# Kernel optimization log

Measured on AMD Instinct MI355X. Metric: run time of the kernel, lower is better.

The kernel has to match this reference:

```python
import jax, jax.numpy as jnp
import numpy as np

N_NODES = 100000
N_EDGES = 400000
IN_DIM, HID, OUT_DIM, NUM_REL = 768, 256, 128, 3


def _init_linear(key, fan_in, fan_out):
    k1, k2 = jax.random.split(key)
    s = 1.0 / np.sqrt(fan_in)
    W = jax.random.uniform(k1, (fan_in, fan_out), jnp.float32, -s, s)
    b = jax.random.uniform(k2, (fan_out,), jnp.float32, -s, s)
    return W, b


def setup_inputs() -> dict:
    key = jax.random.key(0)
    ks = jax.random.split(key, 12)
    x = jax.random.normal(ks[0], (N_NODES, IN_DIM), jnp.float32)
    edge_index = jax.random.randint(ks[1], (2, N_EDGES), 0, N_NODES, jnp.int64 if jax.config.jax_enable_x64 else jnp.int32).astype(jnp.int32)
    edge_type = jax.random.randint(ks[2], (N_EDGES,), 0, NUM_REL).astype(jnp.int32)
    W1, b1 = _init_linear(ks[3], IN_DIM, HID)
    s = 1.0 / np.sqrt(HID)
    conv1_W = jax.random.uniform(ks[4], (NUM_REL, HID, HID), jnp.float32, -s, s)
    conv1_root = jax.random.uniform(ks[5], (HID, HID), jnp.float32, -s, s)
    conv1_bias = jnp.zeros((HID,), jnp.float32)
    conv2_W = jax.random.uniform(ks[6], (NUM_REL, HID, HID), jnp.float32, -s, s)
    conv2_root = jax.random.uniform(ks[7], (HID, HID), jnp.float32, -s, s)
    conv2_bias = jnp.zeros((HID,), jnp.float32)
    W2, b2 = _init_linear(ks[8], HID, OUT_DIM)
    Wc, bc = _init_linear(ks[9], OUT_DIM, 2)
    return {"x": x, "edge_index": edge_index, "edge_type": edge_type,
            "batch_size": 1024,
            "W1": W1, "b1": b1,
            "conv1_W": conv1_W, "conv1_root": conv1_root, "conv1_bias": conv1_bias,
            "conv2_W": conv2_W, "conv2_root": conv2_root, "conv2_bias": conv2_bias,
            "W2": W2, "b2": b2, "Wc": Wc, "bc": bc}


def rgcn_conv(h, src, dst, edge_type, W, root, bias):
    # PyG RGCNConv: mean aggregation per relation + root transform + bias
    n = h.shape[0]
    hs = h[src]                                   # [E, HID] gather
    out = h @ root + bias                         # root/self term
    for r in range(NUM_REL):                      # fixed small relation count
        w = (edge_type == r).astype(h.dtype)      # [E]
        msg = (hs @ W[r]) * w[:, None]            # per-relation transform
        ssum = jax.ops.segment_sum(msg, dst, num_segments=n)
        cnt = jax.ops.segment_sum(w, dst, num_segments=n)
        out = out + ssum / jnp.maximum(cnt, 1.0)[:, None]
    return out


def reference(x, edge_index, edge_type, batch_size,
              W1, b1, conv1_W, conv1_root, conv1_bias,
              conv2_W, conv2_root, conv2_bias, W2, b2, Wc, bc):
    src, dst = edge_index[0], edge_index[1]
    h = jax.nn.relu(x @ W1 + b1)                  # linear1 + ReLU
    h = rgcn_conv(h, src, dst, edge_type, conv1_W, conv1_root, conv1_bias)
    # dropout: identity at inference
    h = rgcn_conv(h, src, dst, edge_type, conv2_W, conv2_root, conv2_bias)
    h = jax.nn.relu(h @ W2 + b2)                  # linear2 + ReLU
    logits = h @ Wc + bc                          # classifier
    return logits[:batch_size]
```

## Files before the change

### kernel.cpp

```cpp
#include <hip/hip_runtime.h>


#define N_NODES 100000
#define N_EDGES 400000
#define IN_DIM  768
#define HID     256
#define OUT_DIM 128
#define NREL    3
#define BATCH   1024
#define KCAT    1024
#define MSGW    768
#define CAP0    32768
#define CAP1    8192
#define ECAP1   32768
#define ECAP2   8192

typedef __attribute__((ext_vector_type(8))) short bf16x8;
typedef __attribute__((ext_vector_type(4))) float f32x4;

static __device__ __forceinline__ int imin(int a, int b) { return a < b ? a : b; }

static __device__ __forceinline__ unsigned short f2bf(float f) {
    union { float f; unsigned int u; } v; v.f = f;
    unsigned int r = v.u + 0x7FFFu + ((v.u >> 16) & 1u);
    return (unsigned short)(r >> 16);
}

__global__ __launch_bounds__(256) void zero_prep(
    uint4* __restrict__ zp, int nz,
    const float* __restrict__ W1,
    const float* __restrict__ c1root, const float* __restrict__ c1W,
    const float* __restrict__ c2root, const float* __restrict__ c2W,
    unsigned short* __restrict__ w1s,
    unsigned short* __restrict__ B1s,
    unsigned short* __restrict__ B2s)
{
    int t = blockIdx.x * blockDim.x + threadIdx.x;
    if (t < nz) { zp[t] = make_uint4(0u, 0u, 0u, 0u); return; }
    int u = t - nz;
    const int P1 = (IN_DIM * HID) / 8;
    const int P2 = (KCAT * HID) / 8;
    unsigned int pk[4];
    if (u < P1) {
        int base = u * 8;
        int j0 = base & 31, c = (base >> 5) & 255, s = base >> 13;
        #pragma unroll
        for (int q = 0; q < 4; q++) {
            unsigned short lo = f2bf(W1[((s * 32 + j0 + 2 * q) << 8) + c]);
            unsigned short hi = f2bf(W1[((s * 32 + j0 + 2 * q + 1) << 8) + c]);
            pk[q] = (unsigned int)lo | ((unsigned int)hi << 16);
        }
        *(uint4*)&w1s[base] = make_uint4(pk[0], pk[1], pk[2], pk[3]);
    } else if (u < P1 + 2 * P2) {
        int which2 = (u - P1) >= P2;
        const float* root = which2 ? c2root : c1root;
        const float* Wr   = which2 ? c2W : c1W;
        unsigned short* dst = which2 ? B2s : B1s;
        int base = ((u - P1) - (which2 ? P2 : 0)) * 8;
        int j0 = base & 31, c = (base >> 5) & 255, s = base >> 13;
        int k0 = s * 32 + j0;
        #pragma unroll
        for (int q = 0; q < 4; q++) {
            int ka = k0 + 2 * q, kb = ka + 1;
            float va = (ka < HID) ? root[(ka << 8) + c] : Wr[((ka - HID) << 8) + c];
            float vb = (kb < HID) ? root[(kb << 8) + c] : Wr[((kb - HID) << 8) + c];
            pk[q] = (unsigned int)f2bf(va) | ((unsigned int)f2bf(vb) << 16);
        }
        *(uint4*)&dst[base] = make_uint4(pk[0], pk[1], pk[2], pk[3]);
    }
}


__global__ void mark1c(const int* __restrict__ ei, int* __restrict__ need1,
                       int* __restrict__ elist2, int* __restrict__ ectr2) {
    int e = blockIdx.x * blockDim.x + threadIdx.x;
    if (e >= N_EDGES) return;
    if (ei[N_EDGES + e] < BATCH) {
        need1[ei[e]] = 1;
        int p = atomicAdd(ectr2, 1);
        if (p < ECAP2) elist2[p] = e;
    }
}

__global__ void mark0c(const int* __restrict__ ei, const int* __restrict__ need1,
                       int* __restrict__ need0,
                       int* __restrict__ elist1, int* __restrict__ ectr1) {
    int e = blockIdx.x * blockDim.x + threadIdx.x;
    if (e >= N_EDGES) return;
    int d = ei[N_EDGES + e];
    if (d < BATCH || need1[d]) {
        need0[ei[e]] = 1;
        int p = atomicAdd(ectr1, 1);
        if (p < ECAP1) elist1[p] = e;
    }
}

__global__ void compact_both(const int* __restrict__ need1, const int* __restrict__ need0,
                             int* __restrict__ idx1, int* __restrict__ map1, int* __restrict__ n1ctr,
                             int* __restrict__ idx0, int* __restrict__ map0, int* __restrict__ n0ctr) {
    int i = blockIdx.x * blockDim.x + threadIdx.x;
    if (i >= N_NODES) return;
    int f1 = (i < BATCH) | need1[i];
    int f0 = f1 | need0[i];
    if (f1) {
        int p = atomicAdd(n1ctr, 1);
        if (p < CAP1) { idx1[p] = i; map1[i] = p; } else map1[i] = -1;
    } else map1[i] = -1;
    if (f0) {
        int p = atomicAdd(n0ctr, 1);
        if (p < CAP0) { idx0[p] = i; map0[i] = p; } else map0[i] = -1;
    } else map0[i] = -1;
}

__global__ void scatter_c(const int* __restrict__ ei, const int* __restrict__ et,
                          const int* __restrict__ elist, const int* __restrict__ ectr, int ecap,
                          const int* __restrict__ mapSrc, const int* __restrict__ mapDst,
                          const float* __restrict__ hsrc,
                          float* __restrict__ Amsg, float* __restrict__ cnt,
                          int cntStride) {
    int g = blockIdx.x * blockDim.x + threadIdx.x;
    int ii = g >> 6, lane = g & 63;
    int n = imin(*ectr, ecap);
    if (ii >= n) return;
    int e = elist[ii];
    int d = ei[N_EDGES + e];
    int row = mapDst ? mapDst[d] : d;
    if (row < 0) return;
    int s = mapSrc[ei[e]];
    if (s < 0) return;
    int r = et[e];
    float4 v = *(const float4*)(hsrc + (size_t)s * HID + lane * 4);
    float* dp = Amsg + (size_t)row * MSGW + (size_t)r * HID + lane * 4;
    atomicAdd(dp + 0, v.x);
    atomicAdd(dp + 1, v.y);
    atomicAdd(dp + 2, v.z);
    atomicAdd(dp + 3, v.w);
    if (lane == 0) atomicAdd(cnt + (size_t)r * cntStride + row, 1.0f);
}

__global__ __launch_bounds__(256) void gemm1_mfma(
    const float* __restrict__ x, const int* __restrict__ idx0,
    const unsigned short* __restrict__ w1s, const float* __restrict__ b1,
    float* __restrict__ h0c, const int* __restrict__ Mptr, int Mcap)
{
    int M = imin(*Mptr, Mcap);
    int bm = blockIdx.x * 64;
    if (bm >= M) return;

    __shared__ unsigned short As[64][40];
    __shared__ unsigned short Bs[256][40];

    int tid = threadIdx.x;
    int w = tid >> 6, lane = tid & 63;
    int l16 = lane & 15, lhi = lane >> 4;

    int ar = tid >> 2, ac = tid & 3;
    int gr = idx0[imin(bm + ar, M - 1)];
    const float* aptr = x + (size_t)gr * IN_DIM + ac * 8;

    f32x4 acc[16];
    #pragma unroll
    for (int i = 0; i < 16; i++) acc[i] = (f32x4)0.0f;

    for (int k0 = 0; k0 < IN_DIM; k0 += 32) {
        float4 a0 = *(const float4*)(aptr + k0);
        float4 a1 = *(const float4*)(aptr + k0 + 4);
        unsigned int p0 = (unsigned int)f2bf(a0.x) | ((unsigned int)f2bf(a0.y) << 16);
        unsigned int p1 = (unsigned int)f2bf(a0.z) | ((unsigned int)f2bf(a0.w) << 16);
        unsigned int p2 = (unsigned int)f2bf(a1.x) | ((unsigned int)f2bf(a1.y) << 16);
        unsigned int p3 = (unsigned int)f2bf(a1.z) | ((unsigned int)f2bf(a1.w) << 16);
        *(uint4*)&As[ar][ac * 8] = make_uint4(p0, p1, p2, p3);

        const uint4* bsrc = (const uint4*)(w1s + ((size_t)(k0 >> 5) * 256 + tid) * 32);
        int bswz = (tid >> 3) & 3;
        uint4 b0 = bsrc[0], b1v = bsrc[1], b2 = bsrc[2], b3 = bsrc[3];
        *(uint4*)&Bs[tid][(0 ^ bswz) * 8] = b0;
        *(uint4*)&Bs[tid][(1 ^ bswz) * 8] = b1v;
        *(uint4*)&Bs[tid][(2 ^ bswz) * 8] = b2;
        *(uint4*)&Bs[tid][(3 ^ bswz) * 8] = b3;
        __syncthreads();

        bf16x8 af = *(bf16x8*)&As[w * 16 + l16][lhi * 8];
        #pragma unroll
        for (int f = 0; f < 16; f++) {
            int col = f * 16 + l16;
            bf16x8 bf = *(bf16x8*)&Bs[col][(lhi ^ ((col >> 3) & 3)) * 8];
            acc[f] = __builtin_amdgcn_mfma_f32_16x16x32_bf16(af, bf, acc[f], 0, 0, 0);
        }
        __syncthreads();
    }

    #pragma unroll
    for (int f = 0; f < 16; f++) {
        int col = f * 16 + l16;
        float bb = b1[col];
        #pragma unroll
        for (int reg = 0; reg < 4; reg++) {
            int row = bm + w * 16 + lhi * 4 + reg;
            if (row < M) h0c[(size_t)row * HID + col] = fmaxf(acc[f][reg] + bb, 0.0f);
        }
    }
}

__global__ __launch_bounds__(256) void conv_mfma(
    const float* __restrict__ hsrc,
    const int* __restrict__ idx, const int* __restrict__ map,
    const float* __restrict__ Amsg,
    const float* __restrict__ cnt, int cntStride,
    const unsigned short* __restrict__ Bt, const float* __restrict__ bias,
    float* __restrict__ Cout, const int* __restrict__ Mptr, int Mcap)
{
    int M = Mptr ? imin(*Mptr, Mcap) : Mcap;
    int bm = blockIdx.x * 64;
    if (bm >= M) return;

    __shared__ unsigned short As[64][40];
    __shared__ unsigned short Bs[256][40];

    int tid = threadIdx.x;
    int w = tid >> 6, lane = tid & 63;
    int l16 = lane & 15, lhi = lane >> 4;

    int ar = tid >> 2, ac = tid & 3;
    int row = imin(bm + ar, M - 1);
    int node = idx ? idx[row] : row;
    int grow = map[node]; if (grow < 0) grow = 0;
    const float* rootp = hsrc + (size_t)grow * HID + ac * 8;
    const float* msgp  = Amsg + (size_t)row * MSGW + ac * 8;
    float sc[NREL];
    #pragma unroll
    for (int r = 0; r < NREL; r++)
        sc[r] = 1.0f / fmaxf(cnt[(size_t)r * cntStride + row], 1.0f);

    f32x4 acc[16];
    #pragma unroll
    for (int i = 0; i < 16; i++) acc[i] = (f32x4)0.0f;

    for (int k0 = 0; k0 < KCAT; k0 += 32) {
        float4 a0, a1;
        if (k0 < HID) {
            a0 = *(const float4*)(rootp + k0);
            a1 = *(const float4*)(rootp + k0 + 4);
        } else {
            float s = sc[(k0 - HID) >> 8];
            a0 = *(const float4*)(msgp + (k0 - HID));
            a1 = *(const float4*)(msgp + (k0 - HID) + 4);
            a0.x *= s; a0.y *= s; a0.z *= s; a0.w *= s;
            a1.x *= s; a1.y *= s; a1.z *= s; a1.w *= s;
        }
        unsigned int p0 = (unsigned int)f2bf(a0.x) | ((unsigned int)f2bf(a0.y) << 16);
        unsigned int p1 = (unsigned int)f2bf(a0.z) | ((unsigned int)f2bf(a0.w) << 16);
        unsigned int p2 = (unsigned int)f2bf(a1.x) | ((unsigned int)f2bf(a1.y) << 16);
        unsigned int p3 = (unsigned int)f2bf(a1.z) | ((unsigned int)f2bf(a1.w) << 16);
        *(uint4*)&As[ar][ac * 8] = make_uint4(p0, p1, p2, p3);

        const uint4* bsrc = (const uint4*)(Bt + ((size_t)(k0 >> 5) * 256 + tid) * 32);
        int bswz = (tid >> 3) & 3;
        uint4 b0 = bsrc[0], b1v = bsrc[1], b2 = bsrc[2], b3 = bsrc[3];
        *(uint4*)&Bs[tid][(0 ^ bswz) * 8] = b0;
        *(uint4*)&Bs[tid][(1 ^ bswz) * 8] = b1v;
        *(uint4*)&Bs[tid][(2 ^ bswz) * 8] = b2;
        *(uint4*)&Bs[tid][(3 ^ bswz) * 8] = b3;
        __syncthreads();

        bf16x8 af = *(bf16x8*)&As[w * 16 + l16][lhi * 8];
        #pragma unroll
        for (int f = 0; f < 16; f++) {
            int col = f * 16 + l16;
            bf16x8 bf = *(bf16x8*)&Bs[col][(lhi ^ ((col >> 3) & 3)) * 8];
            acc[f] = __builtin_amdgcn_mfma_f32_16x16x32_bf16(af, bf, acc[f], 0, 0, 0);
        }
        __syncthreads();
    }

    #pragma unroll
    for (int f = 0; f < 16; f++) {
        int col = f * 16 + l16;
        float bb = bias[col];
        #pragma unroll
        for (int reg = 0; reg < 4; reg++) {
            int r = bm + w * 16 + lhi * 4 + reg;
            if (r < M) Cout[(size_t)r * HID + col] = acc[f][reg] + bb;
        }
    }
}

__global__ __launch_bounds__(256) void lin2_cls(
    const float* __restrict__ h2, const float* __restrict__ W2,
    const float* __restrict__ b2, const float* __restrict__ Wc,
    const float* __restrict__ bc, float* __restrict__ out)
{
    __shared__ float As[16][36];
    __shared__ float Bs[16][132];

    int tid = threadIdx.x;
    int bm = blockIdx.x * 32;
    int tx = tid & 15, ty = tid >> 4;
    int brow = tid >> 4, bch = tid & 15;

    float acc[2][8] = {};

    for (int k0 = 0; k0 < HID; k0 += 16) {
        if (tid < 128) {
            int arow = tid >> 2, ach = tid & 3;
            float4 av = *(const float4*)(h2 + (size_t)(bm + arow) * HID + k0 + ach * 4);
            As[ach * 4 + 0][arow] = av.x;
            As[ach * 4 + 1][arow] = av.y;
            As[ach * 4 + 2][arow] = av.z;
            As[ach * 4 + 3][arow] = av.w;
        }
        const float* bp = W2 + (size_t)(k0 + brow) * OUT_DIM;
        *(float4*)&Bs[brow][bch * 4]      = *(const float4*)(bp + bch * 4);
        *(float4*)&Bs[brow][64 + bch * 4] = *(const float4*)(bp + 64 + bch * 4);
        __syncthreads();
        #pragma unroll
        for (int k = 0; k < 16; k++) {
            float a0 = As[k][ty * 2], a1 = As[k][ty * 2 + 1];
            float4 b0 = *(const float4*)&Bs[k][tx * 8];
            float4 b1 = *(const float4*)&Bs[k][tx * 8 + 4];
            acc[0][0] += a0 * b0.x; acc[0][1] += a0 * b0.y; acc[0][2] += a0 * b0.z; acc[0][3] += a0 * b0.w;
            acc[0][4] += a0 * b1.x; acc[0][5] += a0 * b1.y; acc[0][6] += a0 * b1.z; acc[0][7] += a0 * b1.w;
            acc[1][0] += a1 * b0.x; acc[1][1] += a1 * b0.y; acc[1][2] += a1 * b0.z; acc[1][3] += a1 * b0.w;
            acc[1][4] += a1 * b1.x; acc[1][5] += a1 * b1.y; acc[1][6] += a1 * b1.z; acc[1][7] += a1 * b1.w;
        }
        __syncthreads();
    }

    float s0[2] = {0.f, 0.f}, s1[2] = {0.f, 0.f};
    #pragma unroll
    for (int j = 0; j < 8; j++) {
        int col = tx * 8 + j;
        float w0 = Wc[col * 2 + 0], w1 = Wc[col * 2 + 1];
        float bb = b2[col];
        #pragma unroll
        for (int i = 0; i < 2; i++) {
            float h = fmaxf(acc[i][j] + bb, 0.0f);
            s0[i] += h * w0;
            s1[i] += h * w1;
        }
    }
    #pragma unroll
    for (int o = 1; o <= 8; o <<= 1) {
        #pragma unroll
        for (int i = 0; i < 2; i++) {
            s0[i] += __shfl_xor(s0[i], o);
            s1[i] += __shfl_xor(s1[i], o);
        }
    }
    if (tx == 0) {
        #pragma unroll
        for (int i = 0; i < 2; i++) {
            int row = bm + ty * 2 + i;
            out[row * 2 + 0] = s0[i] + bc[0];
            out[row * 2 + 1] = s1[i] + bc[1];
        }
    }
}


extern "C" void kernel_launch(void* const* d_in, const int* in_sizes, int n_in,
                              void* d_out, int out_size, void* d_ws, size_t ws_size,
                              hipStream_t stream) {
    const float* x      = (const float*)d_in[0];
    const int*   ei     = (const int*)d_in[1];
    const int*   et     = (const int*)d_in[2];
    const float* W1     = (const float*)d_in[4];
    const float* b1     = (const float*)d_in[5];
    const float* c1W    = (const float*)d_in[6];
    const float* c1root = (const float*)d_in[7];
    const float* c1bias = (const float*)d_in[8];
    const float* c2W    = (const float*)d_in[9];
    const float* c2root = (const float*)d_in[10];
    const float* c2bias = (const float*)d_in[11];
    const float* W2     = (const float*)d_in[12];
    const float* b2     = (const float*)d_in[13];
    const float* Wc     = (const float*)d_in[14];
    const float* bc     = (const float*)d_in[15];
    float* out = (float*)d_out;

    char* ws = (char*)d_ws;
    size_t off = 0;
    auto alloc = [&](size_t bytes) -> char* {
        char* p = ws + off;
        off = (off + bytes + 255) & ~(size_t)255;
        return p;
    };

    size_t zb_ctr   = 16;
    size_t zb_cnt1  = (size_t)NREL * CAP1 * 4;
    size_t zb_cnt2  = (size_t)NREL * BATCH * 4;
    size_t zb_need  = (size_t)N_NODES * 4;
    size_t zb_amsg1 = (size_t)CAP1 * MSGW * 4;
    size_t zb_amsg2 = (size_t)BATCH * MSGW * 4;
    size_t zbytes = zb_ctr + zb_cnt1 + zb_cnt2 + 2 * zb_need + zb_amsg1 + zb_amsg2;
    char* zblock = alloc(zbytes);
    int*   n1ctr = (int*)zblock;
    int*   n0ctr = n1ctr + 1;
    int*   ectr1 = n1ctr + 2;
    int*   ectr2 = n1ctr + 3;
    float* cnt1  = (float*)(zblock + zb_ctr);
    float* cnt2  = (float*)(zblock + zb_ctr + zb_cnt1);
    int*   need1 = (int*)(zblock + zb_ctr + zb_cnt1 + zb_cnt2);
    int*   need0 = (int*)((char*)need1 + zb_need);
    float* Amsg1 = (float*)((char*)need0 + zb_need);
    float* Amsg2 = (float*)((char*)Amsg1 + zb_amsg1);

    int* map1  = (int*)alloc(N_NODES * 4);
    int* map0  = (int*)alloc(N_NODES * 4);
    int* idx1  = (int*)alloc(CAP1 * 4);
    int* idx0  = (int*)alloc(CAP0 * 4);
    int* elist1 = (int*)alloc(ECAP1 * 4);
    int* elist2 = (int*)alloc(ECAP2 * 4);
    float* h0c = (float*)alloc((size_t)CAP0 * HID * 4);
    float* h1c = (float*)alloc((size_t)CAP1 * HID * 4);
    float* h2  = (float*)alloc((size_t)BATCH * HID * 4);
    unsigned short* w1s = (unsigned short*)alloc((size_t)IN_DIM * HID * 2);
    unsigned short* B1s = (unsigned short*)alloc((size_t)KCAT * HID * 2);
    unsigned short* B2s = (unsigned short*)alloc((size_t)KCAT * HID * 2);
    (void)ws_size; (void)in_sizes; (void)n_in; (void)out_size;

    const int NB = 256;
    dim3 nodeGrid((N_NODES + NB - 1) / NB);
    dim3 edgeGrid((N_EDGES + NB - 1) / NB);

    int nz = (int)((zbytes + 15) / 16);
    int prep_threads = (IN_DIM * HID) / 8 + 2 * (KCAT * HID) / 8;
    int zp_total = nz + prep_threads;

    zero_prep<<<dim3((zp_total + NB - 1) / NB), NB, 0, stream>>>(
        (uint4*)zblock, nz, W1, c1root, c1W, c2root, c2W, w1s, B1s, B2s);
    mark1c<<<edgeGrid, NB, 0, stream>>>(ei, need1, elist2, ectr2);
    mark0c<<<edgeGrid, NB, 0, stream>>>(ei, need1, need0, elist1, ectr1);
    compact_both<<<nodeGrid, NB, 0, stream>>>(need1, need0, idx1, map1, n1ctr, idx0, map0, n0ctr);
    gemm1_mfma<<<dim3(CAP0 / 64), NB, 0, stream>>>(x, idx0, w1s, b1, h0c, n0ctr, CAP0);
    scatter_c<<<dim3(ECAP1 * 64 / NB), NB, 0, stream>>>(ei, et, elist1, ectr1, ECAP1,
                                                        map0, map1, h0c, Amsg1, cnt1, CAP1);
    conv_mfma<<<dim3(CAP1 / 64), NB, 0, stream>>>(h0c, idx1, map0, Amsg1, cnt1, CAP1,
                                                  B1s, c1bias, h1c, n1ctr, CAP1);
    scatter_c<<<dim3(ECAP2 * 64 / NB), NB, 0, stream>>>(ei, et, elist2, ectr2, ECAP2,
                                                        map1, nullptr, h1c, Amsg2, cnt2, BATCH);
    conv_mfma<<<dim3(BATCH / 64), NB, 0, stream>>>(h1c, nullptr, map1, Amsg2, cnt2, BATCH,
                                                   B2s, c2bias, h2, nullptr, BATCH);
    lin2_cls<<<dim3(BATCH / 32), NB, 0, stream>>>(h2, W2, b2, Wc, bc, out);
}
```

Baseline: 408.6 us.

## Fuse all stages into one persistent kernel with software grid barriers

Replaces the ten separate kernel launches with a single persistent "mega" kernel. It uses grid-stride loops and atomic-counter grid barriers between stages, sized at 256 or 512 blocks from an occupancy query, and falls back to the separate kernels if that query fails. The aim is to remove launch overhead and the idle gaps between small dependent kernels. In exchange it pays for the spin barriers, runs with fewer concurrent blocks for the large gemm and scatter phases, and risks deadlock if the grid is not fully resident. A spin cap breaks out of the barrier after a timeout, which could let a stage start before the previous one finishes.

Result: slower. 471.6 us (+15.4%).

```diff
diff --git a/kernel.cpp b/kernel.cpp
--- a/kernel.cpp
+++ b/kernel.cpp
@@ -14,6 +14,7 @@
 #define CAP1    8192
 #define ECAP1   32768
 #define ECAP2   8192
+#define NBAR    12
 
 typedef __attribute__((ext_vector_type(8))) short bf16x8;
 typedef __attribute__((ext_vector_type(4))) float f32x4;
@@ -26,134 +27,104 @@
     return (unsigned short)(r >> 16);
 }
 
-__global__ __launch_bounds__(256) void zero_prep(
-    uint4* __restrict__ zp, int nz,
-    const float* __restrict__ W1,
-    const float* __restrict__ c1root, const float* __restrict__ c1W,
-    const float* __restrict__ c2root, const float* __restrict__ c2W,
-    unsigned short* __restrict__ w1s,
-    unsigned short* __restrict__ B1s,
-    unsigned short* __restrict__ B2s)
-{
-    int t = blockIdx.x * blockDim.x + threadIdx.x;
-    if (t < nz) { zp[t] = make_uint4(0u, 0u, 0u, 0u); return; }
-    int u = t - nz;
-    const int P1 = (IN_DIM * HID) / 8;
-    const int P2 = (KCAT * HID) / 8;
-    unsigned int pk[4];
-    if (u < P1) {
-        int base = u * 8;
-        int j0 = base & 31, c = (base >> 5) & 255, s = base >> 13;
-        #pragma unroll
-        for (int q = 0; q < 4; q++) {
-            unsigned short lo = f2bf(W1[((s * 32 + j0 + 2 * q) << 8) + c]);
-            unsigned short hi = f2bf(W1[((s * 32 + j0 + 2 * q + 1) << 8) + c]);
-            pk[q] = (unsigned int)lo | ((unsigned int)hi << 16);
-        }
-        *(uint4*)&w1s[base] = make_uint4(pk[0], pk[1], pk[2], pk[3]);
-    } else if (u < P1 + 2 * P2) {
-        int which2 = (u - P1) >= P2;
-        const float* root = which2 ? c2root : c1root;
-        const float* Wr   = which2 ? c2W : c1W;
-        unsigned short* dst = which2 ? B2s : B1s;
-        int base = ((u - P1) - (which2 ? P2 : 0)) * 8;
-        int j0 = base & 31, c = (base >> 5) & 255, s = base >> 13;
-        int k0 = s * 32 + j0;
-        #pragma unroll
-        for (int q = 0; q < 4; q++) {
-            int ka = k0 + 2 * q, kb = ka + 1;
-            float va = (ka < HID) ? root[(ka << 8) + c] : Wr[((ka - HID) << 8) + c];
-            float vb = (kb < HID) ? root[(kb << 8) + c] : Wr[((kb - HID) << 8) + c];
-            pk[q] = (unsigned int)f2bf(va) | ((unsigned int)f2bf(vb) << 16);
-        }
-        *(uint4*)&dst[base] = make_uint4(pk[0], pk[1], pk[2], pk[3]);
-    }
-}
-
-
-__global__ void mark1c(const int* __restrict__ ei, int* __restrict__ need1,
-                       int* __restrict__ elist2, int* __restrict__ ectr2) {
-    int e = blockIdx.x * blockDim.x + threadIdx.x;
-    if (e >= N_EDGES) return;
-    if (ei[N_EDGES + e] < BATCH) {
-        need1[ei[e]] = 1;
-        int p = atomicAdd(ectr2, 1);
-        if (p < ECAP2) elist2[p] = e;
-    }
-}
-
-__global__ void mark0c(const int* __restrict__ ei, const int* __restrict__ need1,
-                       int* __restrict__ need0,
-                       int* __restrict__ elist1, int* __restrict__ ectr1) {
-    int e = blockIdx.x * blockDim.x + threadIdx.x;
-    if (e >= N_EDGES) return;
-    int d = ei[N_EDGES + e];
-    if (d < BATCH || need1[d]) {
-        need0[ei[e]] = 1;
-        int p = atomicAdd(ectr1, 1);
-        if (p < ECAP1) elist1[p] = e;
-    }
-}
-
-__global__ void compact_both(const int* __restrict__ need1, const int* __restrict__ need0,
-                             int* __restrict__ idx1, int* __restrict__ map1, int* __restrict__ n1ctr,
-                             int* __restrict__ idx0, int* __restrict__ map0, int* __restrict__ n0ctr) {
-    int i = blockIdx.x * blockDim.x + threadIdx.x;
-    if (i >= N_NODES) return;
-    int f1 = (i < BATCH) | need1[i];
-    int f0 = f1 | need0[i];
-    if (f1) {
-        int p = atomicAdd(n1ctr, 1);
-        if (p < CAP1) { idx1[p] = i; map1[i] = p; } else map1[i] = -1;
-    } else map1[i] = -1;
-    if (f0) {
-        int p = atomicAdd(n0ctr, 1);
-        if (p < CAP0) { idx0[p] = i; map0[i] = p; } else map0[i] = -1;
-    } else map0[i] = -1;
-}
-
-__global__ void scatter_c(const int* __restrict__ ei, const int* __restrict__ et,
-                          const int* __restrict__ elist, const int* __restrict__ ectr, int ecap,
-                          const int* __restrict__ mapSrc, const int* __restrict__ mapDst,
-                          const float* __restrict__ hsrc,
-                          float* __restrict__ Amsg, float* __restrict__ cnt,
-                          int cntStride) {
-    int g = blockIdx.x * blockDim.x + threadIdx.x;
-    int ii = g >> 6, lane = g & 63;
+struct Prm {
+    const float* x; const int* ei; const int* et;
+    const float *W1, *b1, *c1W, *c1root, *c1bias, *c2W, *c2root, *c2bias, *W2, *b2, *Wc, *bc;
+    float* out;
+    uint4* zp; int nz;
+    int* bar;
+    int *need1, *need0, *map1, *map0, *idx1, *idx0, *elist1, *elist2;
+    int *n1ctr, *n0ctr, *ectr1, *ectr2;
+    float *cnt1, *cnt2, *Amsg1, *Amsg2, *h0c, *h1c, *h2;
+    unsigned short *w1s, *B1s, *B2s;
+};
+
+static __device__ __forceinline__ void gbar(int* bar, int slot) {
+    __syncthreads();
+    if (threadIdx.x == 0) {
+        int* c = bar + slot * 16;
+        __threadfence();
+        atomicAdd(c, 1);
+        int nb = (int)gridDim.x;
+        long spins = 0;
+        while (__hip_atomic_load(c, __ATOMIC_ACQUIRE, __HIP_MEMORY_SCOPE_AGENT) < nb) {
+            __builtin_amdgcn_s_sleep(2);
+            if (++spins > (1L << 24)) break;
+        }
+        __threadfence();
+    }
+    __syncthreads();
+}
+
+
+static __device__ void weight_prep_dev(const Prm& p, int gtid, int gstr) {
+    const int P1n = (IN_DIM * HID) / 8, P2n = (KCAT * HID) / 8;
+    for (int u = gtid; u < P1n + 2 * P2n; u += gstr) {
+        unsigned int pk[4];
+        if (u < P1n) {
+            int base = u * 8;
+            int j0 = base & 31, c = (base >> 5) & 255, s = base >> 13;
+            #pragma unroll
+            for (int q = 0; q < 4; q++) {
+                unsigned short lo = f2bf(p.W1[((s * 32 + j0 + 2 * q) << 8) + c]);
+                unsigned short hi = f2bf(p.W1[((s * 32 + j0 + 2 * q + 1) << 8) + c]);
+                pk[q] = (unsigned int)lo | ((unsigned int)hi << 16);
+            }
+            *(uint4*)&p.w1s[base] = make_uint4(pk[0], pk[1], pk[2], pk[3]);
+        } else {
+            int which2 = (u - P1n) >= P2n;
+            const float* root = which2 ? p.c2root : p.c1root;
+            const float* Wr   = which2 ? p.c2W : p.c1W;
+            unsigned short* dst = which2 ? p.B2s : p.B1s;
+            int base = ((u - P1n) - (which2 ? P2n : 0)) * 8;
+            int j0 = base & 31, c = (base >> 5) & 255, s = base >> 13;
+            int k0 = s * 32 + j0;
+            #pragma unroll
+            for (int q = 0; q < 4; q++) {
+                int ka = k0 + 2 * q, kb = ka + 1;
+                float va = (ka < HID) ? root[(ka << 8) + c] : Wr[((ka - HID) << 8) + c];
+                float vb = (kb < HID) ? root[(kb << 8) + c] : Wr[((kb - HID) << 8) + c];
+                pk[q] = (unsigned int)f2bf(va) | ((unsigned int)f2bf(vb) << 16);
+            }
+            *(uint4*)&dst[base] = make_uint4(pk[0], pk[1], pk[2], pk[3]);
+        }
+    }
+}
+
+static __device__ void scatter_dev(const int* __restrict__ ei, const int* __restrict__ et,
+                                   const int* __restrict__ elist, const int* __restrict__ ectr, int ecap,
+                                   const int* __restrict__ mapSrc, const int* __restrict__ mapDst,
+                                   const float* __restrict__ hsrc,
+                                   float* __restrict__ Amsg, float* __restrict__ cnt,
+                                   int cntStride, int gtid, int gstr) {
     int n = imin(*ectr, ecap);
-    if (ii >= n) return;
-    int e = elist[ii];
-    int d = ei[N_EDGES + e];
-    int row = mapDst ? mapDst[d] : d;
-    if (row < 0) return;
-    int s = mapSrc[ei[e]];
-    if (s < 0) return;
-    int r = et[e];
-    float4 v = *(const float4*)(hsrc + (size_t)s * HID + lane * 4);
-    float* dp = Amsg + (size_t)row * MSGW + (size_t)r * HID + lane * 4;
-    atomicAdd(dp + 0, v.x);
-    atomicAdd(dp + 1, v.y);
-    atomicAdd(dp + 2, v.z);
-    atomicAdd(dp + 3, v.w);
-    if (lane == 0) atomicAdd(cnt + (size_t)r * cntStride + row, 1.0f);
-}
-
-__global__ __launch_bounds__(256) void gemm1_mfma(
-    const float* __restrict__ x, const int* __restrict__ idx0,
-    const unsigned short* __restrict__ w1s, const float* __restrict__ b1,
-    float* __restrict__ h0c, const int* __restrict__ Mptr, int Mcap)
-{
-    int M = imin(*Mptr, Mcap);
-    int bm = blockIdx.x * 64;
-    if (bm >= M) return;
-
-    __shared__ unsigned short As[64][40];
-    __shared__ unsigned short Bs[256][40];
-
+    int tot = n * 64;
+    for (int g = gtid; g < tot; g += gstr) {
+        int ii = g >> 6, lane = g & 63;
+        int e = elist[ii];
+        int d = ei[N_EDGES + e];
+        int row = mapDst ? mapDst[d] : d;
+        if (row < 0) continue;
+        int s = mapSrc[ei[e]];
+        if (s < 0) continue;
+        int r = et[e];
+        float4 v = *(const float4*)(hsrc + (size_t)s * HID + lane * 4);
+        float* dp = Amsg + (size_t)row * MSGW + (size_t)r * HID + lane * 4;
+        atomicAdd(dp + 0, v.x);
+        atomicAdd(dp + 1, v.y);
+        atomicAdd(dp + 2, v.z);
+        atomicAdd(dp + 3, v.w);
+        if (lane == 0) atomicAdd(cnt + (size_t)r * cntStride + row, 1.0f);
+    }
+}
+
+static __device__ void gemm1_tile(const float* __restrict__ x, const int* __restrict__ idx0,
+                                  const unsigned short* __restrict__ w1s, const float* __restrict__ b1,
+                                  float* __restrict__ h0c, int bm, int M,
+                                  unsigned short (*As)[40], unsigned short (*Bs)[40]) {
     int tid = threadIdx.x;
     int w = tid >> 6, lane = tid & 63;
     int l16 = lane & 15, lhi = lane >> 4;
-
     int ar = tid >> 2, ac = tid & 3;
     int gr = idx0[imin(bm + ar, M - 1)];
     const float* aptr = x + (size_t)gr * IN_DIM + ac * 8;
@@ -202,25 +173,16 @@
     }
 }
 
-__global__ __launch_bounds__(256) void conv_mfma(
-    const float* __restrict__ hsrc,
-    const int* __restrict__ idx, const int* __restrict__ map,
-    const float* __restrict__ Amsg,
-    const float* __restrict__ cnt, int cntStride,
-    const unsigned short* __restrict__ Bt, const float* __restrict__ bias,
-    float* __restrict__ Cout, const int* __restrict__ Mptr, int Mcap)
-{
-    int M = Mptr ? imin(*Mptr, Mcap) : Mcap;
-    int bm = blockIdx.x * 64;
-    if (bm >= M) return;
-
-    __shared__ unsigned short As[64][40];
-    __shared__ unsigned short Bs[256][40];
-
+static __device__ void conv_tile(const float* __restrict__ hsrc,
+                                 const int* __restrict__ idx, const int* __restrict__ map,
+                                 const float* __restrict__ Amsg,
+                                 const float* __restrict__ cnt, int cntStride,
+                                 const unsigned short* __restrict__ Bt, const float* __restrict__ bias,
+                                 float* __restrict__ Cout, int bm, int M,
+                                 unsigned short (*As)[40], unsigned short (*Bs)[40]) {
     int tid = threadIdx.x;
     int w = tid >> 6, lane = tid & 63;
     int l16 = lane & 15, lhi = lane >> 4;
-
     int ar = tid >> 2, ac = tid & 3;
     int row = imin(bm + ar, M - 1);
     int node = idx ? idx[row] : row;
@@ -285,16 +247,11 @@
     }
 }
 
-__global__ __launch_bounds__(256) void lin2_cls(
-    const float* __restrict__ h2, const float* __restrict__ W2,
-    const float* __restrict__ b2, const float* __restrict__ Wc,
-    const float* __restrict__ bc, float* __restrict__ out)
-{
-    __shared__ float As[16][36];
-    __shared__ float Bs[16][132];
-
+static __device__ void lin2_tile(const float* __restrict__ h2, const float* __restrict__ W2,
+                                 const float* __restrict__ b2, const float* __restrict__ Wc,
+                                 const float* __restrict__ bc, float* __restrict__ out, int bm,
+                                 float (*Asf)[36], float (*Bsf)[132]) {
     int tid = threadIdx.x;
-    int bm = blockIdx.x * 32;
     int tx = tid & 15, ty = tid >> 4;
     int brow = tid >> 4, bch = tid & 15;
 
@@ -304,20 +261,20 @@
         if (tid < 128) {
             int arow = tid >> 2, ach = tid & 3;
             float4 av = *(const float4*)(h2 + (size_t)(bm + arow) * HID + k0 + ach * 4);
-            As[ach * 4 + 0][arow] = av.x;
-            As[ach * 4 + 1][arow] = av.y;
-            As[ach * 4 + 2][arow] = av.z;
-            As[ach * 4 + 3][arow] = av.w;
+            Asf[ach * 4 + 0][arow] = av.x;
+            Asf[ach * 4 + 1][arow] = av.y;
+            Asf[ach * 4 + 2][arow] = av.z;
+            Asf[ach * 4 + 3][arow] = av.w;
         }
         const float* bp = W2 + (size_t)(k0 + brow) * OUT_DIM;
-        *(float4*)&Bs[brow][bch * 4]      = *(const float4*)(bp + bch * 4);
-        *(float4*)&Bs[brow][64 + bch * 4] = *(const float4*)(bp + 64 + bch * 4);
+        *(float4*)&Bsf[brow][bch * 4]      = *(const float4*)(bp + bch * 4);
+        *(float4*)&Bsf[brow][64 + bch * 4] = *(const float4*)(bp + 64 + bch * 4);
         __syncthreads();
         #pragma unroll
         for (int k = 0; k < 16; k++) {
-            float a0 = As[k][ty * 2], a1 = As[k][ty * 2 + 1];
-            float4 b0 = *(const float4*)&Bs[k][tx * 8];
-            float4 b1 = *(const float4*)&Bs[k][tx * 8 + 4];
+            float a0 = Asf[k][ty * 2], a1 = Asf[k][ty * 2 + 1];
+            float4 b0 = *(const float4*)&Bsf[k][tx * 8];
+            float4 b1 = *(const float4*)&Bsf[k][tx * 8 + 4];
             acc[0][0] += a0 * b0.x; acc[0][1] += a0 * b0.y; acc[0][2] += a0 * b0.z; acc[0][3] += a0 * b0.w;
             acc[0][4] += a0 * b1.x; acc[0][5] += a0 * b1.y; acc[0][6] += a0 * b1.z; acc[0][7] += a0 * b1.w;
             acc[1][0] += a1 * b0.x; acc[1][1] += a1 * b0.y; acc[1][2] += a1 * b0.z; acc[1][3] += a1 * b0.w;
@@ -358,33 +315,201 @@
 }
 
 
+__global__ __launch_bounds__(256, 2) void mega(Prm p) {
+    __shared__ __align__(16) char sm[(64 * 40 + 256 * 40) * 2];
+    unsigned short (*As)[40] = (unsigned short(*)[40])sm;
+    unsigned short (*Bs)[40] = (unsigned short(*)[40])(sm + 64 * 40 * 2);
+
+    const int tid  = threadIdx.x;
+    const int gtid = blockIdx.x * 256 + tid;
+    const int gstr = gridDim.x * 256;
+
+    {
+        uint4 z = make_uint4(0u, 0u, 0u, 0u);
+        for (int t = gtid; t < p.nz; t += gstr) p.zp[t] = z;
+        weight_prep_dev(p, gtid, gstr);
+    }
+    gbar(p.bar, 0);
+
+    for (int e = gtid; e < N_EDGES; e += gstr) {
+        if (p.ei[N_EDGES + e] < BATCH) {
+            p.need1[p.ei[e]] = 1;
+            int q = atomicAdd(p.ectr2, 1);
+            if (q < ECAP2) p.elist2[q] = e;
+        }
+    }
+    gbar(p.bar, 1);
+
+    for (int e = gtid; e < N_EDGES; e += gstr) {
+        int d = p.ei[N_EDGES + e];
+        if (d < BATCH || p.need1[d]) {
+            p.need0[p.ei[e]] = 1;
+            int q = atomicAdd(p.ectr1, 1);
+            if (q < ECAP1) p.elist1[q] = e;
+        }
+    }
+    gbar(p.bar, 2);
+
+    for (int i = gtid; i < N_NODES; i += gstr) {
+        int f1 = (i < BATCH) | p.need1[i];
+        int f0 = f1 | p.need0[i];
+        if (f1) {
+            int q = atomicAdd(p.n1ctr, 1);
+            if (q < CAP1) { p.idx1[q] = i; p.map1[i] = q; } else p.map1[i] = -1;
+        } else p.map1[i] = -1;
+        if (f0) {
+            int q = atomicAdd(p.n0ctr, 1);
+            if (q < CAP0) { p.idx0[q] = i; p.map0[i] = q; } else p.map0[i] = -1;
+        } else p.map0[i] = -1;
+    }
+    gbar(p.bar, 3);
+
+    {
+        int M = imin(*p.n0ctr, CAP0);
+        int nt = (M + 63) >> 6;
+        for (int t = blockIdx.x; t < nt; t += gridDim.x)
+            gemm1_tile(p.x, p.idx0, p.w1s, p.b1, p.h0c, t * 64, M, As, Bs);
+    }
+    gbar(p.bar, 4);
+
+    scatter_dev(p.ei, p.et, p.elist1, p.ectr1, ECAP1, p.map0, p.map1, p.h0c,
+                p.Amsg1, p.cnt1, CAP1, gtid, gstr);
+    gbar(p.bar, 5);
+
+    {
+        int M = imin(*p.n1ctr, CAP1);
+        int nt = (M + 63) >> 6;
+        for (int t = blockIdx.x; t < nt; t += gridDim.x)
+            conv_tile(p.h0c, p.idx1, p.map0, p.Amsg1, p.cnt1, CAP1,
+                      p.B1s, p.c1bias, p.h1c, t * 64, M, As, Bs);
+    }
+    gbar(p.bar, 6);
+
+    scatter_dev(p.ei, p.et, p.elist2, p.ectr2, ECAP2, p.map1, nullptr, p.h1c,
+                p.Amsg2, p.cnt2, BATCH, gtid, gstr);
+    gbar(p.bar, 7);
+
+    for (int t = blockIdx.x; t < BATCH / 64; t += gridDim.x)
+        conv_tile(p.h1c, nullptr, p.map1, p.Amsg2, p.cnt2, BATCH,
+                  p.B2s, p.c2bias, p.h2, t * 64, BATCH, As, Bs);
+    gbar(p.bar, 8);
+
+    {
+        float (*Asf)[36]  = (float(*)[36])sm;
+        float (*Bsf)[132] = (float(*)[132])(sm + 16 * 36 * 4);
+        for (int t = blockIdx.x; t < BATCH / 32; t += gridDim.x)
+            lin2_tile(p.h2, p.W2, p.b2, p.Wc, p.bc, p.out, t * 32, Asf, Bsf);
+    }
+}
+
+
+__global__ void fb_zero_prep(Prm p) {
+    int t = blockIdx.x * blockDim.x + threadIdx.x;
+    if (t < p.nz) { p.zp[t] = make_uint4(0u, 0u, 0u, 0u); return; }
+    weight_prep_dev(p, t - p.nz, 1 << 30);
+}
+__global__ void fb_mark1c(Prm p) {
+    int e = blockIdx.x * blockDim.x + threadIdx.x;
+    if (e >= N_EDGES) return;
+    if (p.ei[N_EDGES + e] < BATCH) {
+        p.need1[p.ei[e]] = 1;
+        int q = atomicAdd(p.ectr2, 1);
+        if (q < ECAP2) p.elist2[q] = e;
+    }
+}
+__global__ void fb_mark0c(Prm p) {
+    int e = blockIdx.x * blockDim.x + threadIdx.x;
+    if (e >= N_EDGES) return;
+    int d = p.ei[N_EDGES + e];
+    if (d < BATCH || p.need1[d]) {
+        p.need0[p.ei[e]] = 1;
+        int q = atomicAdd(p.ectr1, 1);
+        if (q < ECAP1) p.elist1[q] = e;
+    }
+}
+__global__ void fb_compact(Prm p) {
+    int i = blockIdx.x * blockDim.x + threadIdx.x;
+    if (i >= N_NODES) return;
+    int f1 = (i < BATCH) | p.need1[i];
+    int f0 = f1 | p.need0[i];
+    if (f1) {
+        int q = atomicAdd(p.n1ctr, 1);
+        if (q < CAP1) { p.idx1[q] = i; p.map1[i] = q; } else p.map1[i] = -1;
+    } else p.map1[i] = -1;
+    if (f0) {
+        int q = atomicAdd(p.n0ctr, 1);
+        if (q < CAP0) { p.idx0[q] = i; p.map0[i] = q; } else p.map0[i] = -1;
+    } else p.map0[i] = -1;
+}
+__global__ __launch_bounds__(256) void fb_gemm1(Prm p) {
+    __shared__ unsigned short As[64][40];
+    __shared__ unsigned short Bs[256][40];
+    int M = imin(*p.n0ctr, CAP0);
+    int bm = blockIdx.x * 64;
+    if (bm >= M) return;
+    gemm1_tile(p.x, p.idx0, p.w1s, p.b1, p.h0c, bm, M, As, Bs);
+}
+__global__ void fb_scatter1(Prm p) {
+    int g = blockIdx.x * blockDim.x + threadIdx.x;
+    scatter_dev(p.ei, p.et, p.elist1, p.ectr1, ECAP1, p.map0, p.map1, p.h0c,
+                p.Amsg1, p.cnt1, CAP1, g, 1 << 30);
+}
+__global__ __launch_bounds__(256) void fb_conv1(Prm p) {
+    __shared__ unsigned short As[64][40];
+    __shared__ unsigned short Bs[256][40];
+    int M = imin(*p.n1ctr, CAP1);
+    int bm = blockIdx.x * 64;
+    if (bm >= M) return;
+    conv_tile(p.h0c, p.idx1, p.map0, p.Amsg1, p.cnt1, CAP1, p.B1s, p.c1bias, p.h1c, bm, M, As, Bs);
+}
+__global__ void fb_scatter2(Prm p) {
+    int g = blockIdx.x * blockDim.x + threadIdx.x;
+    scatter_dev(p.ei, p.et, p.elist2, p.ectr2, ECAP2, p.map1, nullptr, p.h1c,
+                p.Amsg2, p.cnt2, BATCH, g, 1 << 30);
+}
+__global__ __launch_bounds__(256) void fb_conv2(Prm p) {
+    __shared__ unsigned short As[64][40];
+    __shared__ unsigned short Bs[256][40];
+    conv_tile(p.h1c, nullptr, p.map1, p.Amsg2, p.cnt2, BATCH, p.B2s, p.c2bias, p.h2,
+              blockIdx.x * 64, BATCH, As, Bs);
+}
+__global__ __launch_bounds__(256) void fb_lin2(Prm p) {
+    __shared__ float Asf[16][36];
+    __shared__ float Bsf[16][132];
+    lin2_tile(p.h2, p.W2, p.b2, p.Wc, p.bc, p.out, blockIdx.x * 32, Asf, Bsf);
+}
+
+
 extern "C" void kernel_launch(void* const* d_in, const int* in_sizes, int n_in,
                               void* d_out, int out_size, void* d_ws, size_t ws_size,
                               hipStream_t stream) {
-    const float* x      = (const float*)d_in[0];
-    const int*   ei     = (const int*)d_in[1];
-    const int*   et     = (const int*)d_in[2];
-    const float* W1     = (const float*)d_in[4];
-    const float* b1     = (const float*)d_in[5];
-    const float* c1W    = (const float*)d_in[6];
-    const float* c1root = (const float*)d_in[7];
-    const float* c1bias = (const float*)d_in[8];
-    const float* c2W    = (const float*)d_in[9];
-    const float* c2root = (const float*)d_in[10];
-    const float* c2bias = (const float*)d_in[11];
-    const float* W2     = (const float*)d_in[12];
-    const float* b2     = (const float*)d_in[13];
-    const float* Wc     = (const float*)d_in[14];
-    const float* bc     = (const float*)d_in[15];
-    float* out = (float*)d_out;
+    Prm p;
+    p.x      = (const float*)d_in[0];
+    p.ei     = (const int*)d_in[1];
+    p.et     = (const int*)d_in[2];
+    p.W1     = (const float*)d_in[4];
+    p.b1     = (const float*)d_in[5];
+    p.c1W    = (const float*)d_in[6];
+    p.c1root = (const float*)d_in[7];
+    p.c1bias = (const float*)d_in[8];
+    p.c2W    = (const float*)d_in[9];
+    p.c2root = (const float*)d_in[10];
+    p.c2bias = (const float*)d_in[11];
+    p.W2     = (const float*)d_in[12];
+    p.b2     = (const float*)d_in[13];
+    p.Wc     = (const float*)d_in[14];
+    p.bc     = (const float*)d_in[15];
+    p.out    = (float*)d_out;
 
     char* ws = (char*)d_ws;
     size_t off = 0;
     auto alloc = [&](size_t bytes) -> char* {
-        char* p = ws + off;
+        char* q = ws + off;
         off = (off + bytes + 255) & ~(size_t)255;
-        return p;
+        return q;
     };
+
+    p.bar = (int*)alloc(NBAR * 64);
 
     size_t zb_ctr   = 16;
     size_t zb_cnt1  = (size_t)NREL * CAP1 * 4;
@@ -394,52 +519,54 @@
     size_t zb_amsg2 = (size_t)BATCH * MSGW * 4;
     size_t zbytes = zb_ctr + zb_cnt1 + zb_cnt2 + 2 * zb_need + zb_amsg1 + zb_amsg2;
     char* zblock = alloc(zbytes);
-    int*   n1ctr = (int*)zblock;
-    int*   n0ctr = n1ctr + 1;
-    int*   ectr1 = n1ctr + 2;
-    int*   ectr2 = n1ctr + 3;
-    float* cnt1  = (float*)(zblock + zb_ctr);
-    float* cnt2  = (float*)(zblock + zb_ctr + zb_cnt1);
-    int*   need1 = (int*)(zblock + zb_ctr + zb_cnt1 + zb_cnt2);
-    int*   need0 = (int*)((char*)need1 + zb_need);
-    float* Amsg1 = (float*)((char*)need0 + zb_need);
-    float* Amsg2 = (float*)((char*)Amsg1 + zb_amsg1);
-
-    int* map1  = (int*)alloc(N_NODES * 4);
-    int* map0  = (int*)alloc(N_NODES * 4);
-    int* idx1  = (int*)alloc(CAP1 * 4);
-    int* idx0  = (int*)alloc(CAP0 * 4);
-    int* elist1 = (int*)alloc(ECAP1 * 4);
-    int* elist2 = (int*)alloc(ECAP2 * 4);
-    float* h0c = (float*)alloc((size_t)CAP0 * HID * 4);
-    float* h1c = (float*)alloc((size_t)CAP1 * HID * 4);
-    float* h2  = (float*)alloc((size_t)BATCH * HID * 4);
-    unsigned short* w1s = (unsigned short*)alloc((size_t)IN_DIM * HID * 2);
-    unsigned short* B1s = (unsigned short*)alloc((size_t)KCAT * HID * 2);
-    unsigned short* B2s = (unsigned short*)alloc((size_t)KCAT * HID * 2);
+    p.zp    = (uint4*)zblock;
+    p.nz    = (int)((zbytes + 15) / 16);
+    p.n1ctr = (int*)zblock;
+    p.n0ctr = p.n1ctr + 1;
+    p.ectr1 = p.n1ctr + 2;
+    p.ectr2 = p.n1ctr + 3;
+    p.cnt1  = (float*)(zblock + zb_ctr);
+    p.cnt2  = (float*)(zblock + zb_ctr + zb_cnt1);
+    p.need1 = (int*)(zblock + zb_ctr + zb_cnt1 + zb_cnt2);
+    p.need0 = (int*)((char*)p.need1 + zb_need);
+    p.Amsg1 = (float*)((char*)p.need0 + zb_need);
+    p.Amsg2 = (float*)((char*)p.Amsg1 + zb_amsg1);
+
+    p.map1   = (int*)alloc(N_NODES * 4);
+    p.map0   = (int*)alloc(N_NODES * 4);
+    p.idx1   = (int*)alloc(CAP1 * 4);
+    p.idx0   = (int*)alloc(CAP0 * 4);
+    p.elist1 = (int*)alloc(ECAP1 * 4);
+    p.elist2 = (int*)alloc(ECAP2 * 4);
+    p.h0c    = (float*)alloc((size_t)CAP0 * HID * 4);
+    p.h1c    = (float*)alloc((size_t)CAP1 * HID * 4);
+    p.h2     = (float*)alloc((size_t)BATCH * HID * 4);
+    p.w1s    = (unsigned short*)alloc((size_t)IN_DIM * HID * 2);
+    p.B1s    = (unsigned short*)alloc((size_t)KCAT * HID * 2);
+    p.B2s    = (unsigned short*)alloc((size_t)KCAT * HID * 2);
     (void)ws_size; (void)in_sizes; (void)n_in; (void)out_size;
 
-    const int NB = 256;
-    dim3 nodeGrid((N_NODES + NB - 1) / NB);
-    dim3 edgeGrid((N_EDGES + NB - 1) / NB);
-
-    int nz = (int)((zbytes + 15) / 16);
-    int prep_threads = (IN_DIM * HID) / 8 + 2 * (KCAT * HID) / 8;
-    int zp_total = nz + prep_threads;
-
-    zero_prep<<<dim3((zp_total + NB - 1) / NB), NB, 0, stream>>>(
-        (uint4*)zblock, nz, W1, c1root, c1W, c2root, c2W, w1s, B1s, B2s);
-    mark1c<<<edgeGrid, NB, 0, stream>>>(ei, need1, elist2, ectr2);
-    mark0c<<<edgeGrid, NB, 0, stream>>>(ei, need1, need0, elist1, ectr1);
-    compact_both<<<nodeGrid, NB, 0, stream>>>(need1, need0, idx1, map1, n1ctr, idx0, map0, n0ctr);
-    gemm1_mfma<<<dim3(CAP0 / 64), NB, 0, stream>>>(x, idx0, w1s, b1, h0c, n0ctr, CAP0);
-    scatter_c<<<dim3(ECAP1 * 64 / NB), NB, 0, stream>>>(ei, et, elist1, ectr1, ECAP1,
-                                                        map0, map1, h0c, Amsg1, cnt1, CAP1);
-    conv_mfma<<<dim3(CAP1 / 64), NB, 0, stream>>>(h0c, idx1, map0, Amsg1, cnt1, CAP1,
-                                                  B1s, c1bias, h1c, n1ctr, CAP1);
-    scatter_c<<<dim3(ECAP2 * 64 / NB), NB, 0, stream>>>(ei, et, elist2, ectr2, ECAP2,
-                                                        map1, nullptr, h1c, Amsg2, cnt2, BATCH);
-    conv_mfma<<<dim3(BATCH / 64), NB, 0, stream>>>(h1c, nullptr, map1, Amsg2, cnt2, BATCH,
-                                                   B2s, c2bias, h2, nullptr, BATCH);
-    lin2_cls<<<dim3(BATCH / 32), NB, 0, stream>>>(h2, W2, b2, Wc, bc, out);
-}
+    hipMemsetAsync(p.bar, 0, NBAR * 64, stream);
+
+    int occ = 0;
+    hipError_t qe = hipOccupancyMaxActiveBlocksPerMultiprocessor(&occ, mega, 256, 0);
+
+    if (qe == hipSuccess && occ >= 1) {
+        int nblk = (occ >= 2) ? 512 : 256;
+        mega<<<dim3(nblk), dim3(256), 0, stream>>>(p);
+    } else {
+        const int NB = 256;
+        int prep_threads = (IN_DIM * HID) / 8 + 2 * (KCAT * HID) / 8;
+        int zp_total = p.nz + prep_threads;
+        fb_zero_prep<<<dim3((zp_total + NB - 1) / NB), NB, 0, stream>>>(p);
+        fb_mark1c<<<dim3((N_EDGES + NB - 1) / NB), NB, 0, stream>>>(p);
+        fb_mark0c<<<dim3((N_EDGES + NB - 1) / NB), NB, 0, stream>>>(p);
+        fb_compact<<<dim3((N_NODES + NB - 1) / NB), NB, 0, stream>>>(p);
+        fb_gemm1<<<dim3(CAP0 / 64), NB, 0, stream>>>(p);
+        fb_scatter1<<<dim3(ECAP1 * 64 / NB), NB, 0, stream>>>(p);
+        fb_conv1<<<dim3(CAP1 / 64), NB, 0, stream>>>(p);
+        fb_scatter2<<<dim3(ECAP2 * 64 / NB), NB, 0, stream>>>(p);
+        fb_conv2<<<dim3(BATCH / 64), NB, 0, stream>>>(p);
+        fb_lin2<<<dim3(BATCH / 32), NB, 0, stream>>>(p);
+    }
+}
```
